# Optimization experiments

Measured on AMD Instinct MI355X. Metric: run time of the kernel, lower is better.

Reference implementation:

```python
import jax, jax.numpy as jnp
import numpy as np

N_NODES = 100000
N_EDGES = 1600000
N_GRAPHS = 256
D = 128      # d_graph
H = 256      # hidden
VOCAB = 30000
OUT = 2


def setup_inputs() -> dict:
    key = jax.random.key(0)
    ks = jax.random.split(key, 24)
    def lin(k, fin, fout):
        s = 1.0 / np.sqrt(fin)
        kw, kb = jax.random.split(k)
        return (jax.random.uniform(kw, (fin, fout), jnp.float32, -s, s),
                jax.random.uniform(kb, (fout,), jnp.float32, -s, s))
    inp = {
        'feat': jax.random.randint(ks[0], (N_NODES,), 0, VOCAB),
        'src': jax.random.randint(ks[1], (N_EDGES,), 0, N_NODES),
        'dst': jax.random.randint(ks[2], (N_EDGES,), 0, N_NODES),
        'graph_id': jnp.sort(jax.random.randint(ks[3], (N_NODES,), 0, N_GRAPHS)),
        'emb': jax.random.normal(ks[4], (VOCAB, D), jnp.float32),
    }
    # SAGEConv layer 0/1: fc_self + fc_neigh + bias (mean aggregator)
    inp['ws0'], _ = lin(ks[5], D, D)
    inp['wn0'], inp['b0'] = lin(ks[6], D, D)
    inp['ws1'], _ = lin(ks[7], D, D)
    inp['wn1'], inp['b1'] = lin(ks[8], D, D)
    inp['e1_w'], inp['e1_b'] = lin(ks[9], D, H)
    inp['e2_w'], inp['e2_b'] = lin(ks[10], H, H)
    inp['e3_w'], inp['e3_b'] = lin(ks[11], H, H)
    inp['e4_w'], inp['e4_b'] = lin(ks[12], H, H)
    inp['pred_w'], inp['pred_b'] = lin(ks[13], H, OUT)
    return inp


def _sage_mean(h, src, dst, ws, wn, b):
    # gather src features, mean-scatter to dst (DGL SAGEConv 'mean')
    msg = jnp.take(h, src, axis=0)                       # [E, D]
    agg = jax.ops.segment_sum(msg, dst, num_segments=N_NODES)
    deg = jax.ops.segment_sum(jnp.ones((src.shape[0],), h.dtype), dst,
                              num_segments=N_NODES)
    h_neigh = agg / jnp.maximum(deg, 1.0)[:, None]
    return h @ ws + h_neigh @ wn + b


def reference(feat, src, dst, graph_id, emb,
              ws0, wn0, b0, ws1, wn1, b1,
              e1_w, e1_b, e2_w, e2_b, e3_w, e3_b, e4_w, e4_b,
              pred_w, pred_b):
    h = jnp.take(emb, feat, axis=0)                      # [N, D]
    h = jax.nn.relu(_sage_mean(h, src, dst, ws0, wn0, b0))
    h = jax.nn.relu(_sage_mean(h, src, dst, ws1, wn1, b1))
    # dgl.mean_nodes: per-graph mean pool
    gsum = jax.ops.segment_sum(h, graph_id, num_segments=N_GRAPHS)
    gcnt = jax.ops.segment_sum(jnp.ones((N_NODES,), h.dtype), graph_id,
                               num_segments=N_GRAPHS)
    hg = gsum / jnp.maximum(gcnt, 1.0)[:, None]          # [B, D]
    hidden = jax.nn.relu(hg @ e1_w + e1_b)
    h2 = jax.nn.relu(hidden @ e2_w + e2_b)
    h3 = jax.nn.relu(h2 @ e3_w + e3_b)
    h4 = jax.nn.relu(h3 @ e4_w + e4_b)
    y = h4 @ pred_w + pred_b
    return jax.nn.log_softmax(y, axis=1), hidden
```

## Files before the change

kernel.cpp:

```cpp
#include <hip/hip_runtime.h>
#include <hip/hip_bf16.h>
#include <math.h>

#define DF 128
#define HID 256
#define NG 256

typedef __attribute__((ext_vector_type(8))) short s8v;
typedef __attribute__((ext_vector_type(4))) float f32x4;
typedef __attribute__((ext_vector_type(2))) float f32x2;

__device__ __forceinline__ unsigned pack2bf(float lo, float hi){
  unsigned a = __bfloat16_as_ushort(__float2bfloat16(lo));
  unsigned b = __bfloat16_as_ushort(__float2bfloat16(hi));
  return a | (b<<16);
}

__global__ __launch_bounds__(256)
void k_pre0(const float* __restrict__ emb, unsigned* __restrict__ emb_f8, int nvoc,
            const int* __restrict__ dst, int* __restrict__ gb,
            const int* __restrict__ gid, float* __restrict__ gcnt,
            const float* __restrict__ ws0, const float* __restrict__ wn0,
            const float* __restrict__ ws1, const float* __restrict__ wn1,
            unsigned short* __restrict__ wt,
            int N, int E, int NC){
  __shared__ int hist[256];
  const int b = blockIdx.x, t = threadIdx.x;
  if (b < NC){
    int idx = b*256 + t;
    int total = nvoc*(DF/8);
    if (idx<total){
      const float4* e4 = (const float4*)emb;
      float4 v0 = e4[(size_t)idx*2], v1 = e4[(size_t)idx*2+1];
      unsigned w0 = __builtin_amdgcn_cvt_pk_fp8_f32(v0.x, v0.y, 0, false);
      w0 = __builtin_amdgcn_cvt_pk_fp8_f32(v0.z, v0.w, w0, true);
      unsigned w1 = __builtin_amdgcn_cvt_pk_fp8_f32(v1.x, v1.y, 0, false);
      w1 = __builtin_amdgcn_cvt_pk_fp8_f32(v1.z, v1.w, w1, true);
      ((uint2*)emb_f8)[idx] = make_uint2(w0,w1);
    }
  } else if (b < NC+256){
    int bb = b - NC;
    hist[t]=0; __syncthreads();
    for (int i = bb*256+t; i < E; i += 256*256)
      atomicAdd(&hist[dst[i]>>9], 1);
    __syncthreads();
    if (hist[t]) atomicAdd(&gb[t], hist[t]);
  } else if (b < NC+512){
    int bb = b - (NC+256);
    hist[t]=0; __syncthreads();
    for (int i = bb*256+t; i < N; i += 256*256)
      atomicAdd(&hist[gid[i]], 1);
    __syncthreads();
    if (hist[t]) atomicAdd(&gcnt[t], (float)hist[t]);
  } else {
    int bb = b - (NC+512);
    int n = bb & 127;
    int layer = bb >> 7;
    const float* ws = layer? ws1 : ws0;
    const float* wn = layer? wn1 : wn0;
    float v = (t<128)? ws[t*DF+n] : wn[(t-128)*DF+n];
    wt[((size_t)layer*DF + n)*256 + t] = __bfloat16_as_ushort(__float2bfloat16(v));
  }
}

__global__ __launch_bounds__(256)
void k_pre1(const int* __restrict__ feat, const unsigned* __restrict__ emb_f8,
            unsigned* __restrict__ h_f8, int N){
  int idx = blockIdx.x*256 + threadIdx.x;
  int total = N*8;
  if (idx<total){
    int i = idx>>3, c = idx&7;
    ((uint4*)h_f8)[idx] = ((const uint4*)emb_f8)[(size_t)feat[i]*8 + c];
  }
}

__global__ __launch_bounds__(256)
void k_bplace(const int* __restrict__ src, const int* __restrict__ dst,
              const int* __restrict__ gb, int* __restrict__ bcur,
              unsigned* __restrict__ pairs, int E){
  __shared__ int sgb[256];
  __shared__ int hist[256];
  __shared__ int base[256];
  __shared__ int cur[256];
  const int t = threadIdx.x;
  const int CH = (E + gridDim.x - 1)/gridDim.x;
  const int s = blockIdx.x*CH;
  int e = s+CH; if (e>E) e=E;
  if (s>=E) return;
  int v = gb[t];
  sgb[t]=v;
  hist[t]=0;
  __syncthreads();
  for (int o=1;o<256;o<<=1){
    int x = (t>=o)? sgb[t-o] : 0;
    __syncthreads();
    sgb[t]+=x;
    __syncthreads();
  }
  int bstart = sgb[t]-v;
  for (int i=s+t; i<e; i+=256) atomicAdd(&hist[dst[i]>>9],1);
  __syncthreads();
  if (hist[t]){ base[t] = bstart + atomicAdd(&bcur[t],hist[t]); }
  cur[t]=0;
  __syncthreads();
  for (int i=s+t; i<e; i+=256){
    int d = dst[i];
    int bk = d>>9;
    int r = atomicAdd(&cur[bk],1);
    pairs[base[bk]+r] = ((unsigned)src[i]<<9) | (unsigned)(d & 511);
  }
}

__global__ __launch_bounds__(256)
void k_bcsr(const unsigned* __restrict__ pairs, const int* __restrict__ gb,
            int* __restrict__ offs, int* __restrict__ csr, int N, int E){
  __shared__ int sgb[256];
  __shared__ int ncnt[512];
  __shared__ int noff[512];
  __shared__ int sh[256];
  const int t = threadIdx.x;
  const int b = blockIdx.x;
  const int nb0 = b<<9;
  int v = gb[t];
  sgb[t]=v;
  ncnt[t]=0; ncnt[t+256]=0;
  __syncthreads();
  for (int o=1;o<256;o<<=1){
    int x = (t>=o)? sgb[t-o] : 0;
    __syncthreads();
    sgb[t]+=x;
    __syncthreads();
  }
  const int s = sgb[b]-gb[b];
  const int e = sgb[b];
  for (int i=s+t; i<e; i+=256) atomicAdd(&ncnt[pairs[i] & 511u], 1);
  __syncthreads();
  int v0 = ncnt[2*t], v1 = ncnt[2*t+1];
  int vv = v0+v1;
  sh[t]=vv; __syncthreads();
  for (int o=1;o<256;o<<=1){
    int x=(t>=o)?sh[t-o]:0;
    __syncthreads();
    sh[t]+=x;
    __syncthreads();
  }
  int ex = sh[t]-vv;
  noff[2*t]=ex; noff[2*t+1]=ex+v0;
  __syncthreads();
  {
    int n0 = nb0 + t;
    if (n0 < N) offs[n0] = s + noff[t];
    int n1 = nb0 + t + 256;
    if (n1 < N) offs[n1] = s + noff[t+256];
    if (b == gridDim.x-1 && t==0) offs[N] = E;
  }
  ncnt[t]=0; ncnt[t+256]=0;
  __syncthreads();
  for (int i=s+t; i<e; i+=256){
    unsigned p = pairs[i];
    int d = p & 511u;
    int r = atomicAdd(&ncnt[d],1);
    csr[s + noff[d] + r] = (int)(p >> 9);
  }
}

template<int MODE>
__global__ __launch_bounds__(256,8)
void k_sage(const unsigned char* __restrict__ h_in_f8,
            const int* __restrict__ offs, const int* __restrict__ csr,
            const unsigned short* __restrict__ wt,
            const float* __restrict__ bias,
            unsigned char* __restrict__ h_out_f8,
            const int* __restrict__ gid, float* __restrict__ gsum, int N){
  __shared__ __align__(16) unsigned short s_ab[32*256];
  __shared__ int s_gid[32];
  __shared__ float s_tmp[DF];
  const int t = threadIdx.x;
  const int node0 = blockIdx.x*32;
  const uint4* f8r = (const uint4*)h_in_f8;

  if (MODE==1 && t<32) s_gid[t] = (node0+t<N)? gid[node0+t] : -1;

  const int nn = t>>3, c = t&7;
  const int sw = (nn&7)<<4;

  {
    int node = node0+nn;
    uint4 q = make_uint4(0,0,0,0);
    if (node<N) q = f8r[(size_t)node*8 + c];
    f32x2 u; unsigned pk[8];
    u=__builtin_amdgcn_cvt_pk_f32_fp8(q.x,false); pk[0]=pack2bf(u[0],u[1]);
    u=__builtin_amdgcn_cvt_pk_f32_fp8(q.x,true ); pk[1]=pack2bf(u[0],u[1]);
    u=__builtin_amdgcn_cvt_pk_f32_fp8(q.y,false); pk[2]=pack2bf(u[0],u[1]);
    u=__builtin_amdgcn_cvt_pk_f32_fp8(q.y,true ); pk[3]=pack2bf(u[0],u[1]);
    u=__builtin_amdgcn_cvt_pk_f32_fp8(q.z,false); pk[4]=pack2bf(u[0],u[1]);
    u=__builtin_amdgcn_cvt_pk_f32_fp8(q.z,true ); pk[5]=pack2bf(u[0],u[1]);
    u=__builtin_amdgcn_cvt_pk_f32_fp8(q.w,false); pk[6]=pack2bf(u[0],u[1]);
    u=__builtin_amdgcn_cvt_pk_f32_fp8(q.w,true ); pk[7]=pack2bf(u[0],u[1]);
    int byte0 = nn*512 + c*32;
    *(uint4*)((char*)s_ab + ((byte0   )^sw)) = make_uint4(pk[0],pk[1],pk[2],pk[3]);
    *(uint4*)((char*)s_ab + ((byte0+16)^sw)) = make_uint4(pk[4],pk[5],pk[6],pk[7]);
  }

  {
    const int node = node0+nn;
    float a[16];
    #pragma unroll
    for (int j=0;j<16;j++) a[j]=0.f;
    if (node<N){
      int e0=offs[node], e1=offs[node+1];
      int deg = e1-e0;
      if (deg>0){
        #define ACC16(q) { \
          f32x2 u; \
          u=__builtin_amdgcn_cvt_pk_f32_fp8((q).x,false); a[0]+=u[0]; a[1]+=u[1]; \
          u=__builtin_amdgcn_cvt_pk_f32_fp8((q).x,true ); a[2]+=u[0]; a[3]+=u[1]; \
          u=__builtin_amdgcn_cvt_pk_f32_fp8((q).y,false); a[4]+=u[0]; a[5]+=u[1]; \
          u=__builtin_amdgcn_cvt_pk_f32_fp8((q).y,true ); a[6]+=u[0]; a[7]+=u[1]; \
          u=__builtin_amdgcn_cvt_pk_f32_fp8((q).z,false); a[8]+=u[0]; a[9]+=u[1]; \
          u=__builtin_amdgcn_cvt_pk_f32_fp8((q).z,true ); a[10]+=u[0]; a[11]+=u[1]; \
          u=__builtin_amdgcn_cvt_pk_f32_fp8((q).w,false); a[12]+=u[0]; a[13]+=u[1]; \
          u=__builtin_amdgcn_cvt_pk_f32_fp8((q).w,true ); a[14]+=u[0]; a[15]+=u[1]; }
        int e = e0;
        if (e & 1){
          uint4 q0 = f8r[(size_t)csr[e]*8 + c];
          ACC16(q0);
          e++;
        }
        for (; e+2<=e1; e+=2){
          int2 ss = *(const int2*)&csr[e];
          uint4 q0 = f8r[(size_t)ss.x*8 + c];
          uint4 q1 = f8r[(size_t)ss.y*8 + c];
          ACC16(q0); ACC16(q1);
        }
        if (e<e1){
          uint4 q0 = f8r[(size_t)csr[e]*8 + c];
          ACC16(q0);
        }
        #undef ACC16
        float inv = 1.0f/(float)deg;
        #pragma unroll
        for (int j=0;j<16;j++) a[j]*=inv;
      }
    }
    unsigned pk[8];
    #pragma unroll
    for (int j=0;j<8;j++) pk[j] = pack2bf(a[2*j],a[2*j+1]);
    int byte0 = nn*512 + 256 + c*32;
    *(uint4*)((char*)s_ab + ((byte0   )^sw)) = make_uint4(pk[0],pk[1],pk[2],pk[3]);
    *(uint4*)((char*)s_ab + ((byte0+16)^sw)) = make_uint4(pk[4],pk[5],pk[6],pk[7]);
  }

  const int wv = t>>6;
  const int lr = t&15;
  const int kg = (t&63)>>4;
  __syncthreads();

  f32x4 acc00={0,0,0,0}, acc01={0,0,0,0}, acc10={0,0,0,0}, acc11={0,0,0,0};
  const s8v* wt8 = (const s8v*)wt;
  #pragma unroll
  for (int kh=0; kh<2; kh++){
    s8v bfrag[2][4];
    #pragma unroll
    for (int ks=0; ks<4; ks++){
      int kb = (kh*4+ks)*4 + kg;
      bfrag[0][ks] = wt8[(size_t)(wv*32     + lr)*32 + kb];
      bfrag[1][ks] = wt8[(size_t)(wv*32 + 16+ lr)*32 + kb];
    }
    #pragma unroll
    for (int ks=0; ks<4; ks++){
      int cb = (kh*4+ks)*64 + kg*16;
      int r0 = lr, r1 = 16+lr;
      s8v a0 = *(const s8v*)((const char*)s_ab + ((r0*512+cb) ^ ((r0&7)<<4)));
      s8v a1 = *(const s8v*)((const char*)s_ab + ((r1*512+cb) ^ ((r1&7)<<4)));
      acc00 = __builtin_amdgcn_mfma_f32_16x16x32_bf16(a0, bfrag[0][ks], acc00, 0,0,0);
      acc01 = __builtin_amdgcn_mfma_f32_16x16x32_bf16(a0, bfrag[1][ks], acc01, 0,0,0);
      acc10 = __builtin_amdgcn_mfma_f32_16x16x32_bf16(a1, bfrag[0][ks], acc10, 0,0,0);
      acc11 = __builtin_amdgcn_mfma_f32_16x16x32_bf16(a1, bfrag[1][ks], acc11, 0,0,0);
    }
  }
  __syncthreads();

  float* cbuf = (float*)s_ab;
  #pragma unroll
  for (int r=0;r<4;r++){
    int row0 = kg*4 + r;
    cbuf[(row0   )*DF + wv*32      + lr] = acc00[r];
    cbuf[(row0   )*DF + wv*32 + 16 + lr] = acc01[r];
    cbuf[(row0+16)*DF + wv*32      + lr] = acc10[r];
    cbuf[(row0+16)*DF + wv*32 + 16 + lr] = acc11[r];
  }
  __syncthreads();

  if (MODE==0){
    int row = t>>3, c0 = (t&7)*16;
    int node = node0+row;
    if (node<N){
      float x[16];
      #pragma unroll
      for (int j=0;j<16;j++) x[j] = fmaxf(cbuf[row*DF + c0 + j] + bias[c0+j], 0.f);
      unsigned f0 = __builtin_amdgcn_cvt_pk_fp8_f32(x[0], x[1], 0, false);
      f0 = __builtin_amdgcn_cvt_pk_fp8_f32(x[2], x[3], f0, true);
      unsigned f1 = __builtin_amdgcn_cvt_pk_fp8_f32(x[4], x[5], 0, false);
      f1 = __builtin_amdgcn_cvt_pk_fp8_f32(x[6], x[7], f1, true);
      unsigned f2 = __builtin_amdgcn_cvt_pk_fp8_f32(x[8], x[9], 0, false);
      f2 = __builtin_amdgcn_cvt_pk_fp8_f32(x[10], x[11], f2, true);
      unsigned f3 = __builtin_amdgcn_cvt_pk_fp8_f32(x[12], x[13], 0, false);
      f3 = __builtin_amdgcn_cvt_pk_fp8_f32(x[14], x[15], f3, true);
      *(uint4*)&h_out_f8[(size_t)node*DF + c0] = make_uint4(f0,f1,f2,f3);
    }
  } else {
    const int d = t&127, rh = t>>7;
    const float bd = bias[d];
    int segStart = 0;
    while (segStart < 32 && s_gid[segStart] >= 0){
      int g = s_gid[segStart];
      int segEnd = segStart+1;
      while (segEnd < 32 && s_gid[segEnd] == g) segEnd++;
      float p = 0.f;
      for (int r = segStart+rh; r < segEnd; r += 2)
        p += fmaxf(cbuf[r*DF + d] + bd, 0.f);
      if (rh==1) s_tmp[d] = p;
      __syncthreads();
      if (rh==0) atomicAdd(&gsum[g*DF+d], p + s_tmp[d]);
      __syncthreads();
      segStart = segEnd;
    }
  }
}

__global__ __launch_bounds__(256)
void k_head(const float* __restrict__ gsum, const float* __restrict__ gcnt,
            const float* __restrict__ e1w, const float* __restrict__ e1b,
            const float* __restrict__ e2w, const float* __restrict__ e2b,
            const float* __restrict__ e3w, const float* __restrict__ e3b,
            const float* __restrict__ e4w, const float* __restrict__ e4b,
            const float* __restrict__ pw,  const float* __restrict__ pb,
            float* __restrict__ out, float* __restrict__ hidden){
  __shared__ float hg[DF];
  __shared__ float bufA[HID];
  __shared__ float bufB[HID];
  __shared__ float r0[HID], r1[HID];
  const int g = blockIdx.x, t = threadIdx.x;
  if (t<DF) hg[t] = gsum[g*DF+t] / fmaxf(gcnt[g],1.0f);
  __syncthreads();

  float acc = e1b[t];
  for (int k=0;k<DF;++k) acc += hg[k]*e1w[k*HID+t];
  float h1 = fmaxf(acc,0.f);
  hidden[g*HID+t] = h1;
  bufA[t] = h1;
  __syncthreads();

  acc = e2b[t];
  for (int k=0;k<HID;++k) acc += bufA[k]*e2w[k*HID+t];
  bufB[t] = fmaxf(acc,0.f);
  __syncthreads();

  acc = e3b[t];
  for (int k=0;k<HID;++k) acc += bufB[k]*e3w[k*HID+t];
  bufA[t] = fmaxf(acc,0.f);
  __syncthreads();

  acc = e4b[t];
  for (int k=0;k<HID;++k) acc += bufA[k]*e4w[k*HID+t];
  float h4 = fmaxf(acc,0.f);

  r0[t] = h4*pw[t*2+0];
  r1[t] = h4*pw[t*2+1];
  __syncthreads();
  for (int o=128;o>0;o>>=1){
    if (t<o){ r0[t]+=r0[t+o]; r1[t]+=r1[t+o]; }
    __syncthreads();
  }
  if (t==0){
    float y0 = r0[0]+pb[0], y1 = r1[0]+pb[1];
    float m = fmaxf(y0,y1);
    float l = m + logf(expf(y0-m)+expf(y1-m));
    out[g*2+0]=y0-l;
    out[g*2+1]=y1-l;
  }
}

extern "C" void kernel_launch(void* const* d_in, const int* in_sizes, int n_in,
                              void* d_out, int out_size, void* d_ws, size_t ws_size,
                              hipStream_t stream){
  const int* feat = (const int*)d_in[0];
  const int* src  = (const int*)d_in[1];
  const int* dst  = (const int*)d_in[2];
  const int* gid  = (const int*)d_in[3];
  const float* emb = (const float*)d_in[4];
  const float* ws0 = (const float*)d_in[5];
  const float* wn0 = (const float*)d_in[6];
  const float* b0  = (const float*)d_in[7];
  const float* ws1 = (const float*)d_in[8];
  const float* wn1 = (const float*)d_in[9];
  const float* b1  = (const float*)d_in[10];
  const float* e1w = (const float*)d_in[11];
  const float* e1b = (const float*)d_in[12];
  const float* e2w = (const float*)d_in[13];
  const float* e2b = (const float*)d_in[14];
  const float* e3w = (const float*)d_in[15];
  const float* e3b = (const float*)d_in[16];
  const float* e4w = (const float*)d_in[17];
  const float* e4b = (const float*)d_in[18];
  const float* pw  = (const float*)d_in[19];
  const float* pb  = (const float*)d_in[20];
  const int N = in_sizes[0];
  const int E = in_sizes[1];
  const int nvoc = in_sizes[4] / DF;

  char* basep = (char*)d_ws;
  size_t off=0;
  auto alloc=[&](size_t bytes)->void*{
    void* p = basep+off; off=(off+bytes+255)&~(size_t)255; return p;
  };
  unsigned char*  hA_f8 = (unsigned char*) alloc((size_t)N*DF);
  unsigned char*  hB_f8 = (unsigned char*) alloc((size_t)N*DF);
  unsigned char*  emb_f8= (unsigned char*) alloc((size_t)nvoc*DF);
  int*   offs  = (int*)  alloc((size_t)(N+1)*4);
  int*   csr   = (int*)  alloc((size_t)E*4);
  int*   gb    = (int*)  alloc(1024);
  int*   bcur  = (int*)  alloc(1024);
  unsigned short* wtb = (unsigned short*)alloc((size_t)2*DF*256*2);
  float* gsum  = (float*)alloc((size_t)NG*DF*4);
  float* gcnt  = (float*)alloc((size_t)NG*4);
  unsigned* pairs = (unsigned*)alloc((size_t)E*4);
  float* out    = (float*)d_out;
  float* hidden = out + NG*2;

  hipMemsetAsync(gb, 0, 1024, stream);
  hipMemsetAsync(bcur, 0, 1024, stream);
  hipMemsetAsync(gsum, 0, (size_t)NG*DF*4, stream);
  hipMemsetAsync(gcnt, 0, (size_t)NG*4, stream);

  const int NBK = (N+511)>>9;
  const int NC = (nvoc*(DF/8) + 255)/256;
  k_pre0<<<NC+768,256,0,stream>>>(emb,(unsigned*)emb_f8,nvoc,
                                  dst,gb,gid,gcnt,
                                  ws0,wn0,ws1,wn1,wtb,N,E,NC);
  k_pre1<<<(N*8+255)/256,256,0,stream>>>(feat,(const unsigned*)emb_f8,
                                         (unsigned*)hA_f8,N);
  k_bplace<<<256,256,0,stream>>>(src,dst,gb,bcur,pairs,E);
  k_bcsr<<<NBK,256,0,stream>>>(pairs,gb,offs,csr,N,E);

  k_sage<0><<<(N+31)/32,256,0,stream>>>(hA_f8,offs,csr,wtb,        b0,
                                        hB_f8,nullptr,nullptr,N);
  k_sage<1><<<(N+31)/32,256,0,stream>>>(hB_f8,offs,csr,wtb+DF*256, b1,
                                        nullptr,gid,gsum,N);

  k_head<<<NG,HID,0,stream>>>(gsum,gcnt,e1w,e1b,e2w,e2b,e3w,e3b,e4w,e4b,
                              pw,pb,out,hidden);
}
```

Baseline: 220.8 us.

## Fuse embedding gather with bucket placement and stage CSR indices in LDS

Merges the embedding-gather kernel and the edge bucket-placement kernel into one launch that splits work by block index, removing one launch and letting the two independent jobs run concurrently. In the SAGE kernel, each block cooperatively copies its 32 nodes' CSR neighbor indices into shared memory (up to 1024 entries) before aggregation. The per-lane index loads then read from LDS instead of global memory, with a global fallback when a block's edge count exceeds the cap. This adds 4 KB of LDS per block, which may reduce occupancy at the requested 8 blocks per CU, and adds an extra barrier.

```diff
diff --git a/kernel.cpp b/kernel.cpp
--- a/kernel.cpp
+++ b/kernel.cpp
@@ -5,6 +5,7 @@
 #define DF 128
 #define HID 256
 #define NG 256
+#define CSR_CAP 1024
 
 typedef __attribute__((ext_vector_type(8))) short s8v;
 typedef __attribute__((ext_vector_type(4))) float f32x4;
@@ -64,27 +65,28 @@
 }
 
 __global__ __launch_bounds__(256)
-void k_pre1(const int* __restrict__ feat, const unsigned* __restrict__ emb_f8,
-            unsigned* __restrict__ h_f8, int N){
-  int idx = blockIdx.x*256 + threadIdx.x;
-  int total = N*8;
-  if (idx<total){
-    int i = idx>>3, c = idx&7;
-    ((uint4*)h_f8)[idx] = ((const uint4*)emb_f8)[(size_t)feat[i]*8 + c];
-  }
-}
-
-__global__ __launch_bounds__(256)
-void k_bplace(const int* __restrict__ src, const int* __restrict__ dst,
-              const int* __restrict__ gb, int* __restrict__ bcur,
-              unsigned* __restrict__ pairs, int E){
+void k_mid(const int* __restrict__ feat, const unsigned* __restrict__ emb_f8,
+           unsigned* __restrict__ h_f8, int N,
+           const int* __restrict__ src, const int* __restrict__ dst,
+           const int* __restrict__ gb, int* __restrict__ bcur,
+           unsigned* __restrict__ pairs, int E, int NP1){
+  const int b = blockIdx.x, t = threadIdx.x;
+  if (b < NP1){
+    int idx = b*256 + t;
+    int total = N*8;
+    if (idx<total){
+      int i = idx>>3, c = idx&7;
+      ((uint4*)h_f8)[idx] = ((const uint4*)emb_f8)[(size_t)feat[i]*8 + c];
+    }
+    return;
+  }
   __shared__ int sgb[256];
   __shared__ int hist[256];
   __shared__ int base[256];
   __shared__ int cur[256];
-  const int t = threadIdx.x;
-  const int CH = (E + gridDim.x - 1)/gridDim.x;
-  const int s = blockIdx.x*CH;
+  const int bb = b - NP1;
+  const int CH = (E + 255)/256;
+  const int s = bb*CH;
   int e = s+CH; if (e>E) e=E;
   if (s>=E) return;
   int v = gb[t];
@@ -173,6 +175,7 @@
             unsigned char* __restrict__ h_out_f8,
             const int* __restrict__ gid, float* __restrict__ gsum, int N){
   __shared__ __align__(16) unsigned short s_ab[32*256];
+  __shared__ int s_csr[CSR_CAP];
   __shared__ int s_gid[32];
   __shared__ float s_tmp[DF];
   const int t = threadIdx.x;
@@ -180,6 +183,14 @@
   const uint4* f8r = (const uint4*)h_in_f8;
 
   if (MODE==1 && t<32) s_gid[t] = (node0+t<N)? gid[node0+t] : -1;
+
+  const int eBase = offs[node0];
+  const int eTop  = offs[min(node0+32, N)];
+  const int ecount = eTop - eBase;
+  const bool useLds = (ecount <= CSR_CAP);
+  if (useLds){
+    for (int i=t; i<ecount; i+=256) s_csr[i] = csr[eBase+i];
+  }
 
   const int nn = t>>3, c = t&7;
   const int sw = (nn&7)<<4;
@@ -201,6 +212,7 @@
     *(uint4*)((char*)s_ab + ((byte0   )^sw)) = make_uint4(pk[0],pk[1],pk[2],pk[3]);
     *(uint4*)((char*)s_ab + ((byte0+16)^sw)) = make_uint4(pk[4],pk[5],pk[6],pk[7]);
   }
+  __syncthreads();
 
   {
     const int node = node0+nn;
@@ -221,21 +233,30 @@
           u=__builtin_amdgcn_cvt_pk_f32_fp8((q).z,true ); a[10]+=u[0]; a[11]+=u[1]; \
           u=__builtin_amdgcn_cvt_pk_f32_fp8((q).w,false); a[12]+=u[0]; a[13]+=u[1]; \
           u=__builtin_amdgcn_cvt_pk_f32_fp8((q).w,true ); a[14]+=u[0]; a[15]+=u[1]; }
-        int e = e0;
-        if (e & 1){
-          uint4 q0 = f8r[(size_t)csr[e]*8 + c];
-          ACC16(q0);
-          e++;
-        }
-        for (; e+2<=e1; e+=2){
-          int2 ss = *(const int2*)&csr[e];
-          uint4 q0 = f8r[(size_t)ss.x*8 + c];
-          uint4 q1 = f8r[(size_t)ss.y*8 + c];
-          ACC16(q0); ACC16(q1);
-        }
-        if (e<e1){
-          uint4 q0 = f8r[(size_t)csr[e]*8 + c];
-          ACC16(q0);
+        if (useLds){
+          int le = e0 - eBase, le1 = e1 - eBase;
+          for (; le+2<=le1; le+=2){
+            int s0 = s_csr[le], s1 = s_csr[le+1];
+            uint4 q0 = f8r[(size_t)s0*8 + c];
+            uint4 q1 = f8r[(size_t)s1*8 + c];
+            ACC16(q0); ACC16(q1);
+          }
+          if (le<le1){
+            uint4 q0 = f8r[(size_t)s_csr[le]*8 + c];
+            ACC16(q0);
+          }
+        } else {
+          int e = e0;
+          for (; e+2<=e1; e+=2){
+            int s0 = csr[e], s1 = csr[e+1];
+            uint4 q0 = f8r[(size_t)s0*8 + c];
+            uint4 q1 = f8r[(size_t)s1*8 + c];
+            ACC16(q0); ACC16(q1);
+          }
+          if (e<e1){
+            uint4 q0 = f8r[(size_t)csr[e]*8 + c];
+            ACC16(q0);
+          }
         }
         #undef ACC16
         float inv = 1.0f/(float)deg;
@@ -436,12 +457,13 @@
 
   const int NBK = (N+511)>>9;
   const int NC = (nvoc*(DF/8) + 255)/256;
+  const int NP1 = (N*8 + 255)/256;
   k_pre0<<<NC+768,256,0,stream>>>(emb,(unsigned*)emb_f8,nvoc,
                                   dst,gb,gid,gcnt,
                                   ws0,wn0,ws1,wn1,wtb,N,E,NC);
-  k_pre1<<<(N*8+255)/256,256,0,stream>>>(feat,(const unsigned*)emb_f8,
-                                         (unsigned*)hA_f8,N);
-  k_bplace<<<256,256,0,stream>>>(src,dst,gb,bcur,pairs,E);
+  k_mid<<<NP1+256,256,0,stream>>>(feat,(const unsigned*)emb_f8,
+                                  (unsigned*)hA_f8,N,
+                                  src,dst,gb,bcur,pairs,E,NP1);
   k_bcsr<<<NBK,256,0,stream>>>(pairs,gb,offs,csr,N,E);
 
   k_sage<0><<<(N+31)/32,256,0,stream>>>(hA_f8,offs,csr,wtb,        b0,
```

Measured after the change: 214.6 us. 2.8% less time.
